# Kernel tuning notes

Measured on AMD Instinct MI355X. Metric: run time of the kernel, lower is better.

The kernel has to match this reference:

```python
import jax, jax.numpy as jnp
import numpy as np

TOKENS, D_IN, FEATURES = 8192, 4096, 16384


def setup_inputs() -> dict:
    key = jax.random.key(0)
    k1, k2, k3, k4 = jax.random.split(key, 4)
    inputs = jax.random.normal(k1, (TOKENS, D_IN), dtype=jnp.float32)
    # int4-valued kernel stored as int32 (values in [0, 8) stand in for int4 codes)
    kernel = jax.random.randint(k2, (D_IN, FEATURES), 0, 8, dtype=jnp.int32)
    # per-output-channel scale; keep strictly positive to avoid div-by-zero
    scale = jax.random.uniform(k3, (1, FEATURES), dtype=jnp.float32) + 0.5
    bias = jax.random.normal(k4, (FEATURES,), dtype=jnp.float32)
    return {"inputs": inputs, "kernel": kernel, "scale": scale, "bias": bias}


def reference(inputs, kernel, scale, bias):
    # Dequantize int4 kernel: upcast + per-channel scale division, then GEMM.
    w = kernel.astype(inputs.dtype) / scale          # [D_IN, FEATURES]
    y = inputs @ w                                   # [TOKENS, FEATURES]
    return y + bias
```

## Files before the change

### kernel.cpp

```cpp
#include <hip/hip_runtime.h>

#define TOKENS 8192
#define D_IN   4096
#define FEATS  16384
#define NT     (D_IN / 128)
#define NIT    (NT / 2)

typedef __attribute__((ext_vector_type(4))) int   i4v;
typedef __attribute__((ext_vector_type(4))) float f32x4;

__device__ __forceinline__ void gload_lds16(const void* g, void* l) {
  __builtin_amdgcn_global_load_lds(
      (const __attribute__((address_space(1))) void*)g,
      (__attribute__((address_space(3))) void*)l, 16, 0, 0);
}

__device__ __forceinline__ int pack4(float4 f, float inv) {
  int a = __float2int_rn(f.x * inv), b = __float2int_rn(f.y * inv),
      c = __float2int_rn(f.z * inv), d = __float2int_rn(f.w * inv);
  return (a & 0xff) | ((b & 0xff) << 8) | ((c & 0xff) << 16) | ((d & 0xff) << 24);
}

__global__ __launch_bounds__(256) void quant_x_kernel(const float* __restrict__ x,
                                                      signed char* __restrict__ xq,
                                                      float* __restrict__ xs) {
  const int row = blockIdx.x, t = threadIdx.x;
  const float* xr = x + (long)row * D_IN;
  float4 v0 = *(const float4*)(xr + t * 16 + 0);
  float4 v1 = *(const float4*)(xr + t * 16 + 4);
  float4 v2 = *(const float4*)(xr + t * 16 + 8);
  float4 v3 = *(const float4*)(xr + t * 16 + 12);
  float m = 0.f;
  m = fmaxf(m, fmaxf(fmaxf(fabsf(v0.x), fabsf(v0.y)), fmaxf(fabsf(v0.z), fabsf(v0.w))));
  m = fmaxf(m, fmaxf(fmaxf(fabsf(v1.x), fabsf(v1.y)), fmaxf(fabsf(v1.z), fabsf(v1.w))));
  m = fmaxf(m, fmaxf(fmaxf(fabsf(v2.x), fabsf(v2.y)), fmaxf(fabsf(v2.z), fabsf(v2.w))));
  m = fmaxf(m, fmaxf(fmaxf(fabsf(v3.x), fabsf(v3.y)), fmaxf(fabsf(v3.z), fabsf(v3.w))));
#pragma unroll
  for (int off = 32; off >= 1; off >>= 1) m = fmaxf(m, __shfl_xor(m, off));
  __shared__ float wm[4];
  if ((t & 63) == 0) wm[t >> 6] = m;
  __syncthreads();
  m = fmaxf(fmaxf(wm[0], wm[1]), fmaxf(wm[2], wm[3]));
  m = fmaxf(m, 1e-20f);
  const float inv = 127.f / m;
  if (t == 0) xs[row] = m / 127.f;
  int4 o;
  o.x = pack4(v0, inv); o.y = pack4(v1, inv);
  o.z = pack4(v2, inv); o.w = pack4(v3, inv);
  *(int4*)(xq + (long)row * D_IN + t * 16) = o;
}

__global__ __launch_bounds__(256) void wtrans8_kernel(const int* __restrict__ kq,
                                                      signed char* __restrict__ wt) {
  __shared__ signed char tile[64][68];
  const int n0 = blockIdx.x * 64, k0 = blockIdx.y * 64;
  const int t = threadIdx.x;
  const int kr = t >> 4, nc = (t & 15) * 4;
#pragma unroll
  for (int p = 0; p < 4; p++) {
    int4 v = *(const int4*)(kq + (long)(k0 + kr + 16 * p) * FEATS + n0 + nc);
    tile[kr + 16 * p][nc + 0] = (signed char)v.x;
    tile[kr + 16 * p][nc + 1] = (signed char)v.y;
    tile[kr + 16 * p][nc + 2] = (signed char)v.z;
    tile[kr + 16 * p][nc + 3] = (signed char)v.w;
  }
  __syncthreads();
  const int nr = t >> 4, kc = (t & 15) * 4;
#pragma unroll
  for (int p = 0; p < 4; p++) {
    int n = nr + 16 * p;
    int o = (tile[kc + 0][n] & 0xff) | ((tile[kc + 1][n] & 0xff) << 8) |
            ((tile[kc + 2][n] & 0xff) << 16) | ((tile[kc + 3][n] & 0xff) << 24);
    *(int*)(wt + (long)(n0 + n) * D_IN + k0 + kc) = o;
  }
}

#define BAR        __builtin_amdgcn_s_barrier()
#define WAIT_LGKM  asm volatile("s_waitcnt lgkmcnt(0)" ::: "memory")
#define VMCNT6     asm volatile("s_waitcnt vmcnt(6)" ::: "memory")
#define VMCNT0     asm volatile("s_waitcnt vmcnt(0)" ::: "memory")
#define PRIO1      __builtin_amdgcn_s_setprio(1)
#define PRIO0      __builtin_amdgcn_s_setprio(0)

#define STAGE_A(B_, R0, KT) do { if ((KT) < NT) \
  gload_lds16(Xq + (m0 + (R0) + sr) * (long)D_IN + (long)(KT) * 128 + sgb, \
              (char*)&lds[B_][0][0] + (R0) * 128 + wid * 1024); } while (0)
#define STAGE_B(B_, R0, KT) do { if ((KT) < NT) \
  gload_lds16(Wq + (n0 + (R0) + sr) * (long)D_IN + (long)(KT) * 128 + sgb, \
              (char*)&lds[B_][1][0] + (R0) * 128 + wid * 1024); } while (0)

#define LDA1(B_, I) do { \
  const char* _p = (const char*)&lds[B_][0][0] + (wr * 128 + (I) * 16 + rl) * 128; \
  aF[(I) & 3][0] = *(const i4v*)(_p + koff0); \
  aF[(I) & 3][1] = *(const i4v*)(_p + koff1); } while (0)
#define LDA4(B_, H) do { LDA1(B_, (H)*4+0); LDA1(B_, (H)*4+1); LDA1(B_, (H)*4+2); LDA1(B_, (H)*4+3); } while (0)
#define LDB1(B_, J) do { \
  const char* _p = (const char*)&lds[B_][1][0] + (wc * 64 + (J) * 16 + rl) * 128; \
  bF[J][0] = *(const i4v*)(_p + koff0); \
  bF[J][1] = *(const i4v*)(_p + koff1); } while (0)
#define LDB2(B_, P) do { LDB1(B_, (P)*2+0); LDB1(B_, (P)*2+1); } while (0)

#define MM1(I, J, KS) \
  acc[I][J] = __builtin_amdgcn_mfma_i32_16x16x64_i8(aF[(I) & 3][KS], bF[J][KS], acc[I][J], 0, 0, 0)
#define MM16(H, JH) do { \
  MM1((H)*4+0,(JH)*2+0,0); MM1((H)*4+0,(JH)*2+0,1); \
  MM1((H)*4+0,(JH)*2+1,0); MM1((H)*4+0,(JH)*2+1,1); \
  MM1((H)*4+1,(JH)*2+0,0); MM1((H)*4+1,(JH)*2+0,1); \
  MM1((H)*4+1,(JH)*2+1,0); MM1((H)*4+1,(JH)*2+1,1); \
  MM1((H)*4+2,(JH)*2+0,0); MM1((H)*4+2,(JH)*2+0,1); \
  MM1((H)*4+2,(JH)*2+1,0); MM1((H)*4+2,(JH)*2+1,1); \
  MM1((H)*4+3,(JH)*2+0,0); MM1((H)*4+3,(JH)*2+0,1); \
  MM1((H)*4+3,(JH)*2+1,0); MM1((H)*4+3,(JH)*2+1,1); } while (0)

__global__ __launch_bounds__(512, 2) void gemm8i_kernel(
    const signed char* __restrict__ Xq,
    const signed char* __restrict__ Wq,
    const float* __restrict__ xs,
    const float* __restrict__ scale,
    const float* __restrict__ bias,
    float* __restrict__ C) {
  __shared__ __attribute__((aligned(16))) signed char lds[2][2][256 * 128];

  const int tid = threadIdx.x;
  const int lane = tid & 63, wid = tid >> 6;
  const int wr = wid >> 2, wc = wid & 3;
  const int rl = lane & 15, q = lane >> 4;

  const int bid  = blockIdx.x;
  const int xcd  = bid & 7;
  const int l    = bid >> 3;
  const int rect = l >> 5;
  const int r    = l & 31;
  const int mloc = r & 3;
  const int nl   = r >> 2;
  const long m0 = (long)(xcd * 4 + mloc) * 256;
  const long n0 = (long)(rect * 8 + nl) * 256;

  const int sr = tid >> 3;
  const int sgb = ((tid & 7) ^ (sr & 7)) * 16;

  const int xm = (rl & 7) << 4;
  const int koff0 = (q * 16) ^ xm;
  const int koff1 = (64 + q * 16) ^ xm;

  i4v acc[8][4] = {};
  i4v aF[4][2], bF[4][2];

  STAGE_B(0, 0, 0); STAGE_B(0, 64, 0); STAGE_B(0, 128, 0); STAGE_B(0, 192, 0);
  STAGE_A(0, 0, 0); STAGE_A(0, 64, 0); STAGE_A(0, 128, 0); STAGE_A(0, 192, 0);
  STAGE_B(1, 0, 1); STAGE_B(1, 64, 1); STAGE_B(1, 128, 1); STAGE_B(1, 192, 1);
  STAGE_A(1, 0, 1); STAGE_A(1, 128, 1);
  VMCNT6;
  BAR;

  for (int it = 0; it < NIT; ++it) {
    const int t1 = 2 * it + 1, t2 = 2 * it + 2, t3 = 2 * it + 3;
    LDA4(0, 0); LDB2(0, 0);
    STAGE_A(1, 64, t1); STAGE_A(1, 192, t1);
    WAIT_LGKM; PRIO1; MM16(0, 0); PRIO0; BAR;
    LDB2(0, 1);
    STAGE_A(0, 0, t2); STAGE_A(0, 128, t2);
    WAIT_LGKM; PRIO1; MM16(0, 1); PRIO0; BAR;
    LDA4(0, 1);
    STAGE_B(0, 0, t2); STAGE_B(0, 64, t2);
    WAIT_LGKM; PRIO1; MM16(1, 0); PRIO0; BAR;
    STAGE_B(0, 128, t2); STAGE_B(0, 192, t2);
    PRIO1; MM16(1, 1); PRIO0;
    if (it == NIT - 1) { VMCNT0; } else { VMCNT6; }
    BAR;
    LDA4(1, 0); LDB2(1, 0);
    STAGE_A(0, 64, t2); STAGE_A(0, 192, t2);
    WAIT_LGKM; PRIO1; MM16(0, 0); PRIO0; BAR;
    LDB2(1, 1);
    STAGE_A(1, 0, t3); STAGE_A(1, 128, t3);
    WAIT_LGKM; PRIO1; MM16(0, 1); PRIO0; BAR;
    LDA4(1, 1);
    STAGE_B(1, 0, t3); STAGE_B(1, 64, t3);
    WAIT_LGKM; PRIO1; MM16(1, 0); PRIO0; BAR;
    STAGE_B(1, 128, t3); STAGE_B(1, 192, t3);
    PRIO1; MM16(1, 1); PRIO0;
    VMCNT6;
    BAR;
  }

#pragma unroll
  for (int j = 0; j < 4; j++) {
    const long col = n0 + wc * 64 + j * 16 + rl;
    const float rs = 1.0f / scale[col];
    const float bv = bias[col];
#pragma unroll
    for (int i = 0; i < 8; i++) {
      const long row0 = m0 + wr * 128 + i * 16 + q * 4;
#pragma unroll
      for (int r2 = 0; r2 < 4; r2++) {
        C[(row0 + r2) * (long)FEATS + col] = (float)acc[i][j][r2] * xs[row0 + r2] * rs + bv;
      }
    }
  }
}

__global__ void naive_kernel(const float* __restrict__ x, const int* __restrict__ kq,
                             const float* __restrict__ scale, const float* __restrict__ bias,
                             float* __restrict__ out) {
  __shared__ float xa[16][16];
  __shared__ float wb[16][17];
  const int n = blockIdx.x * 16 + threadIdx.x;
  const int m = blockIdx.y * 16 + threadIdx.y;
  float accv = 0.f;
  for (int k0 = 0; k0 < D_IN; k0 += 16) {
    xa[threadIdx.y][threadIdx.x] = x[(long)m * D_IN + k0 + threadIdx.x];
    wb[threadIdx.y][threadIdx.x] = (float)kq[(long)(k0 + threadIdx.y) * FEATS + n];
    __syncthreads();
#pragma unroll
    for (int kk = 0; kk < 16; kk++) accv += xa[threadIdx.y][kk] * wb[kk][threadIdx.x];
    __syncthreads();
  }
  out[(long)m * FEATS + n] = accv * (1.0f / scale[n]) + bias[n];
}

extern "C" void kernel_launch(void* const* d_in, const int* in_sizes, int n_in,
                              void* d_out, int out_size, void* d_ws, size_t ws_size,
                              hipStream_t stream) {
  const float* x     = (const float*)d_in[0];
  const int*   kq    = (const int*)d_in[1];
  const float* scale = (const float*)d_in[2];
  const float* bias  = (const float*)d_in[3];
  float* out = (float*)d_out;

  const size_t need = (size_t)TOKENS * D_IN + (size_t)FEATS * D_IN + TOKENS * 4;
  if (ws_size < need) {
    naive_kernel<<<dim3(FEATS / 16, TOKENS / 16), dim3(16, 16), 0, stream>>>(
        x, kq, scale, bias, out);
    return;
  }

  signed char* Xq = (signed char*)d_ws;
  signed char* Wq = Xq + (size_t)TOKENS * D_IN;
  float* xs = (float*)(Wq + (size_t)FEATS * D_IN);

  quant_x_kernel<<<TOKENS, 256, 0, stream>>>(x, Xq, xs);
  wtrans8_kernel<<<dim3(FEATS / 64, D_IN / 64), dim3(256), 0, stream>>>(kq, Wq);
  gemm8i_kernel<<<dim3((TOKENS / 256) * (FEATS / 256)), 512, 0, stream>>>(
      Xq, Wq, xs, scale, bias, out);
}
```

Baseline: 691.2 us.

## Stage GEMM epilogue through LDS for coalesced vector stores; drop manual LGKM waits

The epilogue now writes scaled and biased results into a padded LDS buffer that reuses the main-loop tile memory. It then reads them back so each group of lanes writes a contiguous row segment with 16-byte vector stores, replacing the scattered 4-byte output stores. The main loop also loads all B fragments up front and removes the explicit lgkmcnt(0) waits, leaving the compiler to insert LDS waits. The costs are extra barriers and LDS traffic in the epilogue, a slightly larger shared allocation, and possibly less precise scheduling of the LDS waits.

```diff
diff --git a/kernel.cpp b/kernel.cpp
--- a/kernel.cpp
+++ b/kernel.cpp
@@ -76,29 +76,30 @@
 }
 
 #define BAR        __builtin_amdgcn_s_barrier()
-#define WAIT_LGKM  asm volatile("s_waitcnt lgkmcnt(0)" ::: "memory")
 #define VMCNT6     asm volatile("s_waitcnt vmcnt(6)" ::: "memory")
 #define VMCNT0     asm volatile("s_waitcnt vmcnt(0)" ::: "memory")
 #define PRIO1      __builtin_amdgcn_s_setprio(1)
 #define PRIO0      __builtin_amdgcn_s_setprio(0)
 
+#define TILEBASE(B_, MAT) (smem + (B_) * 65536 + (MAT) * 32768)
+
 #define STAGE_A(B_, R0, KT) do { if ((KT) < NT) \
   gload_lds16(Xq + (m0 + (R0) + sr) * (long)D_IN + (long)(KT) * 128 + sgb, \
-              (char*)&lds[B_][0][0] + (R0) * 128 + wid * 1024); } while (0)
+              TILEBASE(B_, 0) + (R0) * 128 + wid * 1024); } while (0)
 #define STAGE_B(B_, R0, KT) do { if ((KT) < NT) \
   gload_lds16(Wq + (n0 + (R0) + sr) * (long)D_IN + (long)(KT) * 128 + sgb, \
-              (char*)&lds[B_][1][0] + (R0) * 128 + wid * 1024); } while (0)
+              TILEBASE(B_, 1) + (R0) * 128 + wid * 1024); } while (0)
 
 #define LDA1(B_, I) do { \
-  const char* _p = (const char*)&lds[B_][0][0] + (wr * 128 + (I) * 16 + rl) * 128; \
+  const char* _p = TILEBASE(B_, 0) + (wr * 128 + (I) * 16 + rl) * 128; \
   aF[(I) & 3][0] = *(const i4v*)(_p + koff0); \
   aF[(I) & 3][1] = *(const i4v*)(_p + koff1); } while (0)
 #define LDA4(B_, H) do { LDA1(B_, (H)*4+0); LDA1(B_, (H)*4+1); LDA1(B_, (H)*4+2); LDA1(B_, (H)*4+3); } while (0)
 #define LDB1(B_, J) do { \
-  const char* _p = (const char*)&lds[B_][1][0] + (wc * 64 + (J) * 16 + rl) * 128; \
+  const char* _p = TILEBASE(B_, 1) + (wc * 64 + (J) * 16 + rl) * 128; \
   bF[J][0] = *(const i4v*)(_p + koff0); \
   bF[J][1] = *(const i4v*)(_p + koff1); } while (0)
-#define LDB2(B_, P) do { LDB1(B_, (P)*2+0); LDB1(B_, (P)*2+1); } while (0)
+#define LDB4(B_) do { LDB1(B_, 0); LDB1(B_, 1); LDB1(B_, 2); LDB1(B_, 3); } while (0)
 
 #define MM1(I, J, KS) \
   acc[I][J] = __builtin_amdgcn_mfma_i32_16x16x64_i8(aF[(I) & 3][KS], bF[J][KS], acc[I][J], 0, 0, 0)
@@ -112,6 +113,9 @@
   MM1((H)*4+3,(JH)*2+0,0); MM1((H)*4+3,(JH)*2+0,1); \
   MM1((H)*4+3,(JH)*2+1,0); MM1((H)*4+3,(JH)*2+1,1); } while (0)
 
+#define EP_PITCH 260
+#define EP_HALF  (64 * EP_PITCH)
+
 __global__ __launch_bounds__(512, 2) void gemm8i_kernel(
     const signed char* __restrict__ Xq,
     const signed char* __restrict__ Wq,
@@ -119,7 +123,7 @@
     const float* __restrict__ scale,
     const float* __restrict__ bias,
     float* __restrict__ C) {
-  __shared__ __attribute__((aligned(16))) signed char lds[2][2][256 * 128];
+  __shared__ __attribute__((aligned(16))) char smem[133120];
 
   const int tid = threadIdx.x;
   const int lane = tid & 63, wid = tid >> 6;
@@ -155,45 +159,68 @@
 
   for (int it = 0; it < NIT; ++it) {
     const int t1 = 2 * it + 1, t2 = 2 * it + 2, t3 = 2 * it + 3;
-    LDA4(0, 0); LDB2(0, 0);
+    LDA4(0, 0); LDB4(0);
     STAGE_A(1, 64, t1); STAGE_A(1, 192, t1);
-    WAIT_LGKM; PRIO1; MM16(0, 0); PRIO0; BAR;
-    LDB2(0, 1);
+    PRIO1; MM16(0, 0); PRIO0; BAR;
     STAGE_A(0, 0, t2); STAGE_A(0, 128, t2);
-    WAIT_LGKM; PRIO1; MM16(0, 1); PRIO0; BAR;
+    PRIO1; MM16(0, 1); PRIO0; BAR;
     LDA4(0, 1);
     STAGE_B(0, 0, t2); STAGE_B(0, 64, t2);
-    WAIT_LGKM; PRIO1; MM16(1, 0); PRIO0; BAR;
+    PRIO1; MM16(1, 0); PRIO0; BAR;
     STAGE_B(0, 128, t2); STAGE_B(0, 192, t2);
     PRIO1; MM16(1, 1); PRIO0;
     if (it == NIT - 1) { VMCNT0; } else { VMCNT6; }
     BAR;
-    LDA4(1, 0); LDB2(1, 0);
+    LDA4(1, 0); LDB4(1);
     STAGE_A(0, 64, t2); STAGE_A(0, 192, t2);
-    WAIT_LGKM; PRIO1; MM16(0, 0); PRIO0; BAR;
-    LDB2(1, 1);
+    PRIO1; MM16(0, 0); PRIO0; BAR;
     STAGE_A(1, 0, t3); STAGE_A(1, 128, t3);
-    WAIT_LGKM; PRIO1; MM16(0, 1); PRIO0; BAR;
+    PRIO1; MM16(0, 1); PRIO0; BAR;
     LDA4(1, 1);
     STAGE_B(1, 0, t3); STAGE_B(1, 64, t3);
-    WAIT_LGKM; PRIO1; MM16(1, 0); PRIO0; BAR;
+    PRIO1; MM16(1, 0); PRIO0; BAR;
     STAGE_B(1, 128, t3); STAGE_B(1, 192, t3);
     PRIO1; MM16(1, 1); PRIO0;
     VMCNT6;
     BAR;
   }
 
+  float rsv[4], bvv[4];
 #pragma unroll
   for (int j = 0; j < 4; j++) {
     const long col = n0 + wc * 64 + j * 16 + rl;
-    const float rs = 1.0f / scale[col];
-    const float bv = bias[col];
-#pragma unroll
-    for (int i = 0; i < 8; i++) {
-      const long row0 = m0 + wr * 128 + i * 16 + q * 4;
-#pragma unroll
-      for (int r2 = 0; r2 < 4; r2++) {
-        C[(row0 + r2) * (long)FEATS + col] = (float)acc[i][j][r2] * xs[row0 + r2] * rs + bv;
+    rsv[j] = 1.0f / scale[col];
+    bvv[j] = bias[col];
+  }
+  float* ldsF = (float*)smem;
+#pragma unroll
+  for (int p = 0; p < 2; ++p) {
+    if (p) BAR;
+#pragma unroll
+    for (int i = 0; i < 4; ++i) {
+      const int ii = p * 4 + i;
+      const long grow0 = m0 + wr * 128 + ii * 16 + q * 4;
+#pragma unroll
+      for (int r2 = 0; r2 < 4; ++r2) {
+        const float xv = xs[grow0 + r2];
+        const int lrow = i * 16 + q * 4 + r2;
+        float* dst = ldsF + wr * EP_HALF + lrow * EP_PITCH;
+#pragma unroll
+        for (int j = 0; j < 4; ++j)
+          dst[wc * 64 + j * 16 + rl] = (float)acc[ii][j][r2] * xv * rsv[j] + bvv[j];
+      }
+    }
+    BAR;
+#pragma unroll
+    for (int h = 0; h < 2; ++h) {
+      const int rr = wid * 8 + (lane >> 3);
+      const long grow = m0 + h * 128 + p * 64 + rr;
+      const float* src = ldsF + h * EP_HALF + rr * EP_PITCH + (lane & 7) * 4;
+      float* crow = C + grow * (long)FEATS + n0 + (lane & 7) * 4;
+#pragma unroll
+      for (int g = 0; g < 8; ++g) {
+        f32x4 v = *(const f32x4*)(src + g * 32);
+        *(f32x4*)(crow + g * 32) = v;
       }
     }
   }
```

New measurement: 612.4 us. 11.4% less time.
